# Optimization experiments

Measured on AMD Instinct MI355X. Metric: run time of the kernel, lower is better.

The kernel has to match this reference:

```python
import jax, jax.numpy as jnp
import numpy as np

# BERT-base geometry
B, N, H, DH = 4, 512, 12, 64
HID = H * DH            # 768
E = 65536               # total edges (~avg degree 32)
NREL = 64               # relation vocabulary


def setup_inputs() -> dict:
    key = jax.random.key(0)
    ks = jax.random.split(key, 12)
    node_states = jax.random.normal(ks[0], (B, N, HID), jnp.float32)
    b = jax.random.randint(ks[1], (E,), 0, B)
    hn = jax.random.randint(ks[2], (E,), 0, N)
    tn = jax.random.randint(ks[3], (E,), 0, N)
    r = jax.random.randint(ks[4], (E,), 0, NREL)
    edge_indices = jnp.stack([b, hn, tn, r]).astype(jnp.int32)  # (4, E)
    node_type_ids = jnp.zeros((B, N), jnp.int32)  # unused by this subclass
    sc = 0.02
    Wq = jax.random.normal(ks[5], (HID, HID), jnp.float32) * sc
    bq = jnp.zeros((HID,), jnp.float32)
    Wk = jax.random.normal(ks[6], (HID, HID), jnp.float32) * sc
    bk = jnp.zeros((HID,), jnp.float32)
    Wv = jax.random.normal(ks[7], (HID, HID), jnp.float32) * sc
    bv = jnp.zeros((HID,), jnp.float32)
    # relation matrix embeddings: one (DH, DH) matrix per relation id
    rel_emb = jnp.eye(DH, dtype=jnp.float32)[None] + jax.random.normal(ks[8], (NREL, DH, DH), jnp.float32) * sc
    return {"node_states": node_states, "edge_indices": edge_indices,
            "node_type_ids": node_type_ids, "Wq": Wq, "bq": bq,
            "Wk": Wk, "bk": bk, "Wv": Wv, "bv": bv, "rel_emb": rel_emb}


def reference(node_states, edge_indices, node_type_ids, Wq, bq, Wk, bk, Wv, bv, rel_emb):
    Bq, Nn, hid = node_states.shape
    # dense QKV projections (torch Linear: y = x @ W^T + b)
    Q = node_states @ Wq.T + bq
    K = node_states @ Wk.T + bk
    V = (node_states @ Wv.T + bv).reshape(Bq, Nn, H, DH)  # (B,N,H,D)
    be, he, te, re = edge_indices  # each (E,)
    # per-edge gathers
    Qe = Q[be, he].reshape(-1, H, DH)   # (E,H,D)
    Ke = K[be, te].reshape(-1, H, DH)   # (E,H,D)
    Re = rel_emb[re]                     # (E,D,D) relation matrix per edge
    # Q projected through relation matrix, then inner product with K per head
    Qp = jnp.einsum('ehd,edk->ehk', Qe, Re)
    logits = jnp.einsum('ehd,ehd->eh', Qp, Ke) / jnp.sqrt(jnp.float32(DH))  # (E,H)
    # sparse softmax over tail nodes: segment = (batch, head_node)
    seg = be * Nn + he
    nseg = Bq * Nn
    m = jax.ops.segment_max(logits, seg, num_segments=nseg)      # (BN,H)
    ex = jnp.exp(logits - m[seg])
    denom = jax.ops.segment_sum(ex, seg, num_segments=nseg)      # (BN,H)
    p = ex / denom[seg]                                          # (E,H)
    # dropout prob = 0.0 (deterministic reference)
    # aggregate: out[b,i,h,:] = sum_edges p_e * V[b, tail_e, h, :]
    contrib = p[:, :, None] * V[be, te]                          # (E,H,D)
    out = jax.ops.segment_sum(contrib, seg, num_segments=nseg)   # (BN,H,D)
    return out.reshape(Bq, Nn, H * DH)
```

## Files before the change

### kernel.cpp

```cpp
#include <hip/hip_runtime.h>
#include <hip/hip_bf16.h>

#define NB   4
#define NN   512
#define NH   12
#define DHD  64
#define HID  768
#define NE   65536
#define NSEG 2048
#define NREL 64
#define NSUB 32
#define NRSUB (NREL * NSUB)
#define LGS  16

typedef short bf16x8 __attribute__((ext_vector_type(8)));
typedef float f32x4  __attribute__((ext_vector_type(4)));

__device__ __forceinline__ unsigned short f2bf(float f) {
    __hip_bfloat16 h = __float2bfloat16(f);
    return *reinterpret_cast<unsigned short*>(&h);
}
__device__ __forceinline__ float bf2f(unsigned short s) {
    return __int_as_float(((int)s) << 16);
}
__device__ __forceinline__ void load_lds16(const void* g, void* l) {
    __builtin_amdgcn_global_load_lds(
        (const __attribute__((address_space(1))) unsigned int*)g,
        (__attribute__((address_space(3))) unsigned int*)l, 16, 0, 0);
}

#define NX4 ((2048 * 768) / 4)
#define NW4 ((768 * 768) / 4)
__global__ __launch_bounds__(256) void cast_kernel(
    const float* __restrict__ X, const float* __restrict__ Wq,
    const float* __restrict__ Wk, const float* __restrict__ Wv,
    unsigned short* __restrict__ Xh, unsigned short* __restrict__ Wh)
{
    const int i = blockIdx.x * 256 + threadIdx.x;
    float4 v;
    ushort4* dst;
    if (i < NX4) {
        v = ((const float4*)X)[i];
        dst = &((ushort4*)Xh)[i];
    } else {
        const int j = i - NX4;
        const float* W = (j < NW4) ? Wq : ((j < 2 * NW4) ? Wk : Wv);
        const int jj = (j < NW4) ? j : ((j < 2 * NW4) ? j - NW4 : j - 2 * NW4);
        v = ((const float4*)W)[jj];
        dst = &((ushort4*)Wh)[j];
    }
    ushort4 r;
    r.x = f2bf(v.x); r.y = f2bf(v.y); r.z = f2bf(v.z); r.w = f2bf(v.w);
    *dst = r;
}

__global__ __launch_bounds__(256) void qkv_mfma(
    const unsigned short* __restrict__ Xh, const unsigned short* __restrict__ Wh,
    const float* __restrict__ bq, const float* __restrict__ bk,
    const float* __restrict__ bv,
    unsigned short* __restrict__ Qh, unsigned short* __restrict__ Kh,
    float* __restrict__ Vo)
{
    const int z = blockIdx.z;
    const unsigned short* W = Wh + (size_t)z * (768 * 768);
    const float* bias = (z == 0) ? bq : ((z == 1) ? bk : bv);

    const int n0 = blockIdx.x * 128;
    const int m0 = blockIdx.y * 128;
    const int tid  = threadIdx.x;
    const int lane = tid & 63;
    const int wave = tid >> 6;
    const int wm = wave >> 1, wn = wave & 1;

    __shared__ unsigned short As[128 * 64];
    __shared__ unsigned short Bs[128 * 64];

    f32x4 acc[4][4];
    #pragma unroll
    for (int a = 0; a < 4; ++a)
        #pragma unroll
        for (int b = 0; b < 4; ++b) acc[a][b] = (f32x4){0.f, 0.f, 0.f, 0.f};

    const int ml = lane & 15;
    const int q4 = lane >> 4;

    for (int k0 = 0; k0 < HID; k0 += 64) {
        __syncthreads();
        #pragma unroll
        for (int l = 0; l < 4; ++l) {
            const int idx = (l * 4 + wave) * 64 + lane;
            const int row = idx >> 3;
            const int kq  = (idx & 7) ^ (row & 7);
            load_lds16(Xh + (size_t)(m0 + row) * HID + k0 + kq * 8,
                       As + (l * 4 + wave) * 512);
            load_lds16(W + (size_t)(n0 + row) * HID + k0 + kq * 8,
                       Bs + (l * 4 + wave) * 512);
        }
        __syncthreads();

        #pragma unroll
        for (int ks = 0; ks < 2; ++ks) {
            bf16x8 af[4], bfr[4];
            #pragma unroll
            for (int t = 0; t < 4; ++t) {
                const int ar = wm * 64 + t * 16 + ml;
                const int ac = (ks * 4 + q4) ^ (ar & 7);
                af[t] = *(const bf16x8*)(As + ar * 64 + ac * 8);
                const int br = wn * 64 + t * 16 + ml;
                const int bc = (ks * 4 + q4) ^ (br & 7);
                bfr[t] = *(const bf16x8*)(Bs + br * 64 + bc * 8);
            }
            #pragma unroll
            for (int mt = 0; mt < 4; ++mt)
                #pragma unroll
                for (int nt = 0; nt < 4; ++nt)
                    acc[mt][nt] = __builtin_amdgcn_mfma_f32_16x16x32_bf16(
                        af[mt], bfr[nt], acc[mt][nt], 0, 0, 0);
        }
    }

    #pragma unroll
    for (int nt = 0; nt < 4; ++nt) {
        const int col = n0 + wn * 64 + nt * 16 + ml;
        const float bcol = bias[col];
        #pragma unroll
        for (int mt = 0; mt < 4; ++mt) {
            const int row = m0 + wm * 64 + mt * 16 + q4 * 4;
            #pragma unroll
            for (int rg = 0; rg < 4; ++rg) {
                const float v = acc[mt][nt][rg] + bcol;
                const size_t o = (size_t)(row + rg) * HID + col;
                if (z == 0)      Qh[o] = f2bf(v);
                else if (z == 1) Kh[o] = f2bf(v);
                else             Vo[o] = v;
            }
        }
    }
}

__global__ void hist_kernel(const int* __restrict__ ei,
                            int* __restrict__ count, int* __restrict__ rcount2)
{
    const int e = blockIdx.x * 256 + threadIdx.x;
    const int b  = ei[e];
    const int hn = ei[NE + e];
    const int rr = ei[3 * NE + e];
    const int sub = (e >> 8) & (NSUB - 1);
    atomicAdd(&count[b * NN + hn], 1);
    atomicAdd(&rcount2[rr * NSUB + sub], 1);
}

__global__ void scan_kernel(const int* __restrict__ cnt, int* __restrict__ ofs)
{
    __shared__ int buf[256];
    const int tid = threadIdx.x;
    int local[8];
    int s = 0;
    #pragma unroll
    for (int i = 0; i < 8; ++i) { local[i] = cnt[tid * 8 + i]; s += local[i]; }
    buf[tid] = s;
    __syncthreads();
    for (int off = 1; off < 256; off <<= 1) {
        const int v = (tid >= off) ? buf[tid - off] : 0;
        __syncthreads();
        buf[tid] += v;
        __syncthreads();
    }
    int run = buf[tid] - s;
    #pragma unroll
    for (int i = 0; i < 8; ++i) { ofs[tid * 8 + i] = run; run += local[i]; }
    if (tid == 255) ofs[2048] = run;
}

__global__ void scatter_kernel(const int* __restrict__ ei, const int* __restrict__ offs,
                               int* __restrict__ cursor,
                               const int* __restrict__ rofs2, int* __restrict__ rcursor2,
                               int* __restrict__ s_te, int* __restrict__ s_seg,
                               int* __restrict__ r_pos)
{
    const int e = blockIdx.x * 256 + threadIdx.x;
    const int b  = ei[e];
    const int hn = ei[NE + e];
    const int tn = ei[2 * NE + e];
    const int rr = ei[3 * NE + e];
    const int sub = (e >> 8) & (NSUB - 1);
    const int seg = b * NN + hn;
    const int pos = offs[seg] + atomicAdd(&cursor[seg], 1);
    s_te[pos]  = tn;
    s_seg[pos] = seg;
    const int rb = rr * NSUB + sub;
    const int rj = atomicAdd(&rcursor2[rb], 1);
    r_pos[rofs2[rb] + rj] = pos;
}

__global__ __launch_bounds__(256) void rel_logits(
    const unsigned short* __restrict__ Qh, const unsigned short* __restrict__ Kh,
    const float* __restrict__ rel,
    const int* __restrict__ rofs2, const int* __restrict__ r_pos,
    const int* __restrict__ s_te, const int* __restrict__ s_seg,
    float* __restrict__ Lg)
{
    const int r = blockIdx.x;
    const int rstart = rofs2[r * NSUB];
    const int rows = (rofs2[(r + 1) * NSUB] - rstart) * NH;
    const int tid = threadIdx.x;
    const int lane = tid & 63;
    const int wave = tid >> 6;

    __shared__ float ReS[64][65];
    __shared__ int qb[256], kb[256], oi[256];
    __shared__ float QpS[4][16][67];

    {
        const float* Rg = rel + (size_t)r * 4096;
        for (int i = tid; i < 1024; i += 256) {
            const float4 v = ((const float4*)Rg)[i];
            const int row = i >> 4, c4 = (i & 15) * 4;
            ReS[row][c4] = v.x; ReS[row][c4 + 1] = v.y;
            ReS[row][c4 + 2] = v.z; ReS[row][c4 + 3] = v.w;
        }
    }
    __syncthreads();

    bf16x8 bfrag[2][4];
    {
        const int q4 = lane >> 4, n = lane & 15;
        #pragma unroll
        for (int ks = 0; ks < 2; ++ks)
            #pragma unroll
            for (int nt = 0; nt < 4; ++nt) {
                bf16x8 f;
                #pragma unroll
                for (int j = 0; j < 8; ++j)
                    f[j] = (short)f2bf(ReS[ks * 32 + q4 * 8 + j][nt * 16 + n]);
                bfrag[ks][nt] = f;
            }
    }

    for (int t0 = blockIdx.y * 256; t0 < rows; t0 += gridDim.y * 256) {
        __syncthreads();
        {
            const int rowid = t0 + tid;
            if (rowid < rows) {
                const int el = rowid / 12;
                const int h  = rowid - el * 12;
                const int pos = r_pos[rstart + el];
                const int seg = s_seg[pos];
                const int te  = s_te[pos];
                const int b   = seg >> 9;
                qb[tid] = seg * HID + h * 64;
                kb[tid] = (b * NN + te) * HID + h * 64;
                oi[tid] = pos * LGS + h;
            } else { qb[tid] = 0; kb[tid] = 0; oi[tid] = -1; }
        }
        __syncthreads();

        for (int g = wave; g < 16; g += 4) {
            const int m = lane & 15, q4 = lane >> 4;
            const int qbase = qb[g * 16 + m];
            f32x4 cfr[4] = {{0,0,0,0},{0,0,0,0},{0,0,0,0},{0,0,0,0}};
            #pragma unroll
            for (int ks = 0; ks < 2; ++ks) {
                const bf16x8 afr = *(const bf16x8*)(Qh + qbase + ks * 32 + q4 * 8);
                #pragma unroll
                for (int nt = 0; nt < 4; ++nt)
                    cfr[nt] = __builtin_amdgcn_mfma_f32_16x16x32_bf16(
                        afr, bfrag[ks][nt], cfr[nt], 0, 0, 0);
            }
            #pragma unroll
            for (int nt = 0; nt < 4; ++nt)
                #pragma unroll
                for (int rg = 0; rg < 4; ++rg)
                    QpS[wave][q4 * 4 + rg][nt * 16 + m] = cfr[nt][rg];

            const int rw = lane >> 2, ch = (lane & 3) * 16;
            const int rowid2 = g * 16 + rw;
            const int kbase = kb[rowid2];
            const bf16x8 k0 = *(const bf16x8*)(Kh + kbase + ch);
            const bf16x8 k1 = *(const bf16x8*)(Kh + kbase + ch + 8);
            float s = 0.f;
            #pragma unroll
            for (int i = 0; i < 8; ++i) {
                s = fmaf(QpS[wave][rw][ch + i],     bf2f((unsigned short)k0[i]), s);
                s = fmaf(QpS[wave][rw][ch + 8 + i], bf2f((unsigned short)k1[i]), s);
            }
            s += __shfl_xor(s, 1, 64);
            s += __shfl_xor(s, 2, 64);
            if ((lane & 3) == 0) {
                const int o = oi[rowid2];
                if (o >= 0) Lg[o] = s * 0.125f;
            }
        }
    }
}

__global__ __launch_bounds__(256) void seg_softmax_agg(
    const float* __restrict__ V, const float* __restrict__ Lg,
    const int* __restrict__ offs, const int* __restrict__ s_te,
    float* __restrict__ out)
{
    const int seg  = blockIdx.x;
    const int tid  = threadIdx.x;
    const int lane = tid & 63;
    const int w    = tid >> 6;
    const int start = offs[seg];
    const int cnt   = offs[seg + 1] - start;
    const int browbase = seg & ~(NN - 1);

    __shared__ int   te_s[64];
    __shared__ float pv[4][3][64];

    float m0 = -1e30f, m1 = -1e30f, m2 = -1e30f;
    float l0 = 0.f, l1 = 0.f, l2 = 0.f;
    float acc0 = 0.f, acc1 = 0.f, acc2 = 0.f;

    for (int c0 = 0; c0 < cnt; c0 += 64) {
        const int cc = min(64, cnt - c0);
        __syncthreads();
        if (tid < cc) te_s[tid] = s_te[start + c0 + tid];
        __syncthreads();

        float g0 = -1e30f, g1 = -1e30f, g2 = -1e30f;
        if (lane < cc) {
            const float* Lp = Lg + (size_t)(start + c0 + lane) * LGS;
            g0 = Lp[w]; g1 = Lp[4 + w]; g2 = Lp[8 + w];
        }
        float x0 = g0, x1 = g1, x2 = g2;
        #pragma unroll
        for (int o = 1; o < 64; o <<= 1) {
            x0 = fmaxf(x0, __shfl_xor(x0, o, 64));
            x1 = fmaxf(x1, __shfl_xor(x1, o, 64));
            x2 = fmaxf(x2, __shfl_xor(x2, o, 64));
        }
        const float nm0 = fmaxf(m0, x0), nm1 = fmaxf(m1, x1), nm2 = fmaxf(m2, x2);
        const float a0 = __expf(m0 - nm0), a1 = __expf(m1 - nm1), a2 = __expf(m2 - nm2);
        float p0 = (lane < cc) ? __expf(g0 - nm0) : 0.f;
        float p1 = (lane < cc) ? __expf(g1 - nm1) : 0.f;
        float p2 = (lane < cc) ? __expf(g2 - nm2) : 0.f;
        float s0 = p0, s1 = p1, s2 = p2;
        #pragma unroll
        for (int o = 1; o < 64; o <<= 1) {
            s0 += __shfl_xor(s0, o, 64);
            s1 += __shfl_xor(s1, o, 64);
            s2 += __shfl_xor(s2, o, 64);
        }
        l0 = l0 * a0 + s0; l1 = l1 * a1 + s1; l2 = l2 * a2 + s2;
        m0 = nm0; m1 = nm1; m2 = nm2;
        pv[w][0][lane] = p0; pv[w][1][lane] = p1; pv[w][2][lane] = p2;

        acc0 *= a0; acc1 *= a1; acc2 *= a2;
        for (int j = 0; j < cc; ++j) {
            const float* __restrict__ Vr =
                V + (size_t)(browbase + te_s[j]) * HID + lane;
            acc0 = fmaf(pv[w][0][j], Vr[w * 64],       acc0);
            acc1 = fmaf(pv[w][1][j], Vr[(4 + w) * 64], acc1);
            acc2 = fmaf(pv[w][2][j], Vr[(8 + w) * 64], acc2);
        }
    }

    float* Yo = out + (size_t)seg * HID;
    Yo[tid]       = (l0 > 0.f) ? acc0 / l0 : 0.f;
    Yo[tid + 256] = (l1 > 0.f) ? acc1 / l1 : 0.f;
    Yo[tid + 512] = (l2 > 0.f) ? acc2 / l2 : 0.f;
}

extern "C" void kernel_launch(void* const* d_in, const int* in_sizes, int n_in,
                              void* d_out, int out_size, void* d_ws, size_t ws_size,
                              hipStream_t stream)
{
    const float* X   = (const float*)d_in[0];
    const int*   EI  = (const int*)d_in[1];
    const float* Wq  = (const float*)d_in[3];
    const float* bq  = (const float*)d_in[4];
    const float* Wk  = (const float*)d_in[5];
    const float* bk  = (const float*)d_in[6];
    const float* Wv  = (const float*)d_in[7];
    const float* bv  = (const float*)d_in[8];
    const float* rel = (const float*)d_in[9];
    float* out = (float*)d_out;

    char* p = (char*)d_ws;
    unsigned short* Qh = (unsigned short*)p;  p += (size_t)NSEG * HID * 2;
    unsigned short* Kh = (unsigned short*)p;  p += (size_t)NSEG * HID * 2;
    float* Vb = (float*)p;                    p += (size_t)NSEG * HID * 4;
    unsigned short* Xh = (unsigned short*)p;
    float* Lg = (float*)p;                    p += (size_t)NE * LGS * 4;
    unsigned short* Wh = (unsigned short*)p;  p += (size_t)3 * 768 * 768 * 2;
    int* offs     = (int*)p;                  p += 2052 * 4;
    int* rofs2    = (int*)p;                  p += (NRSUB + 4) * 4;
    int* count    = (int*)p;                  p += NSEG * 4;
    int* cursor   = (int*)p;                  p += NSEG * 4;
    int* rcount2  = (int*)p;                  p += NRSUB * 4;
    int* rcursor2 = (int*)p;                  p += NRSUB * 4;
    int* s_te     = (int*)p;                  p += NE * 4;
    int* s_seg    = (int*)p;                  p += NE * 4;
    int* r_pos    = (int*)p;                  p += NE * 4;

    cast_kernel<<<(NX4 + 3 * NW4 + 255) / 256, 256, 0, stream>>>(
        X, Wq, Wk, Wv, Xh, Wh);
    qkv_mfma<<<dim3(HID / 128, (NB * NN) / 128, 3), 256, 0, stream>>>(
        Xh, Wh, bq, bk, bv, Qh, Kh, Vb);

    hipMemsetAsync(count, 0, (2 * NSEG + 2 * NRSUB) * sizeof(int), stream);
    hist_kernel<<<NE / 256, 256, 0, stream>>>(EI, count, rcount2);
    scan_kernel<<<1, 256, 0, stream>>>(count, offs);
    scan_kernel<<<1, 256, 0, stream>>>(rcount2, rofs2);
    scatter_kernel<<<NE / 256, 256, 0, stream>>>(EI, offs, cursor, rofs2, rcursor2,
                                                 s_te, s_seg, r_pos);

    rel_logits<<<dim3(NREL, 32), 256, 0, stream>>>(Qh, Kh, rel, rofs2, r_pos,
                                                   s_te, s_seg, Lg);
    seg_softmax_agg<<<NSEG, 256, 0, stream>>>(Vb, Lg, offs, s_te, out);
}
```

Baseline: 188.0 us.

## Fuse bf16 cast into QKV GEMM, merge scans, shuffle-based aggregation, retune grid

Removes the separate fp32-to-bf16 cast kernel and converts X and W tiles to bf16 while staging them into LDS inside the QKV GEMM. This drops a full read/write pass and one launch, but gives up async global_load_lds in favour of register-staged loads. The two scan launches become one two-block launch. The segment-softmax aggregation now broadcasts tail indices and probabilities with wave shuffles instead of LDS plus barriers. The rel_logits grid grows from 32 to 48 y-blocks, and the QpS row padding changes.

```diff
diff --git a/kernel.cpp b/kernel.cpp
--- a/kernel.cpp
+++ b/kernel.cpp
@@ -23,46 +23,18 @@
 __device__ __forceinline__ float bf2f(unsigned short s) {
     return __int_as_float(((int)s) << 16);
 }
-__device__ __forceinline__ void load_lds16(const void* g, void* l) {
-    __builtin_amdgcn_global_load_lds(
-        (const __attribute__((address_space(1))) unsigned int*)g,
-        (__attribute__((address_space(3))) unsigned int*)l, 16, 0, 0);
-}
-
-#define NX4 ((2048 * 768) / 4)
-#define NW4 ((768 * 768) / 4)
-__global__ __launch_bounds__(256) void cast_kernel(
-    const float* __restrict__ X, const float* __restrict__ Wq,
-    const float* __restrict__ Wk, const float* __restrict__ Wv,
-    unsigned short* __restrict__ Xh, unsigned short* __restrict__ Wh)
-{
-    const int i = blockIdx.x * 256 + threadIdx.x;
-    float4 v;
-    ushort4* dst;
-    if (i < NX4) {
-        v = ((const float4*)X)[i];
-        dst = &((ushort4*)Xh)[i];
-    } else {
-        const int j = i - NX4;
-        const float* W = (j < NW4) ? Wq : ((j < 2 * NW4) ? Wk : Wv);
-        const int jj = (j < NW4) ? j : ((j < 2 * NW4) ? j - NW4 : j - 2 * NW4);
-        v = ((const float4*)W)[jj];
-        dst = &((ushort4*)Wh)[j];
-    }
-    ushort4 r;
-    r.x = f2bf(v.x); r.y = f2bf(v.y); r.z = f2bf(v.z); r.w = f2bf(v.w);
-    *dst = r;
-}
 
 __global__ __launch_bounds__(256) void qkv_mfma(
-    const unsigned short* __restrict__ Xh, const unsigned short* __restrict__ Wh,
+    const float* __restrict__ X,
+    const float* __restrict__ Wq, const float* __restrict__ Wk,
+    const float* __restrict__ Wv,
     const float* __restrict__ bq, const float* __restrict__ bk,
     const float* __restrict__ bv,
     unsigned short* __restrict__ Qh, unsigned short* __restrict__ Kh,
     float* __restrict__ Vo)
 {
     const int z = blockIdx.z;
-    const unsigned short* W = Wh + (size_t)z * (768 * 768);
+    const float* W    = (z == 0) ? Wq : ((z == 1) ? Wk : Wv);
     const float* bias = (z == 0) ? bq : ((z == 1) ? bk : bv);
 
     const int n0 = blockIdx.x * 128;
@@ -87,14 +59,29 @@
     for (int k0 = 0; k0 < HID; k0 += 64) {
         __syncthreads();
         #pragma unroll
-        for (int l = 0; l < 4; ++l) {
-            const int idx = (l * 4 + wave) * 64 + lane;
+        for (int i = 0; i < 4; ++i) {
+            const int idx = tid + i * 256;
             const int row = idx >> 3;
-            const int kq  = (idx & 7) ^ (row & 7);
-            load_lds16(Xh + (size_t)(m0 + row) * HID + k0 + kq * 8,
-                       As + (l * 4 + wave) * 512);
-            load_lds16(W + (size_t)(n0 + row) * HID + k0 + kq * 8,
-                       Bs + (l * 4 + wave) * 512);
+            const int c   = idx & 7;
+            const int sl  = c ^ (row & 7);
+            const float* Xg = X + (size_t)(m0 + row) * HID + k0 + c * 8;
+            const float4 a0 = *(const float4*)Xg;
+            const float4 a1 = *(const float4*)(Xg + 4);
+            bf16x8 av;
+            av[0] = (short)f2bf(a0.x); av[1] = (short)f2bf(a0.y);
+            av[2] = (short)f2bf(a0.z); av[3] = (short)f2bf(a0.w);
+            av[4] = (short)f2bf(a1.x); av[5] = (short)f2bf(a1.y);
+            av[6] = (short)f2bf(a1.z); av[7] = (short)f2bf(a1.w);
+            *(bf16x8*)&As[row * 64 + sl * 8] = av;
+            const float* Wg = W + (size_t)(n0 + row) * HID + k0 + c * 8;
+            const float4 b0 = *(const float4*)Wg;
+            const float4 b1 = *(const float4*)(Wg + 4);
+            bf16x8 bv8;
+            bv8[0] = (short)f2bf(b0.x); bv8[1] = (short)f2bf(b0.y);
+            bv8[2] = (short)f2bf(b0.z); bv8[3] = (short)f2bf(b0.w);
+            bv8[4] = (short)f2bf(b1.x); bv8[5] = (short)f2bf(b1.y);
+            bv8[6] = (short)f2bf(b1.z); bv8[7] = (short)f2bf(b1.w);
+            *(bf16x8*)&Bs[row * 64 + sl * 8] = bv8;
         }
         __syncthreads();
 
@@ -150,8 +137,11 @@
     atomicAdd(&rcount2[rr * NSUB + sub], 1);
 }
 
-__global__ void scan_kernel(const int* __restrict__ cnt, int* __restrict__ ofs)
-{
+__global__ void scan2_kernel(const int* __restrict__ cntA, int* __restrict__ ofsA,
+                             const int* __restrict__ cntB, int* __restrict__ ofsB)
+{
+    const int* cnt = blockIdx.x ? cntB : cntA;
+    int* ofs       = blockIdx.x ? ofsB : ofsA;
     __shared__ int buf[256];
     const int tid = threadIdx.x;
     int local[8];
@@ -193,6 +183,7 @@
     r_pos[rofs2[rb] + rj] = pos;
 }
 
+#define RLY 48
 __global__ __launch_bounds__(256) void rel_logits(
     const unsigned short* __restrict__ Qh, const unsigned short* __restrict__ Kh,
     const float* __restrict__ rel,
@@ -209,7 +200,7 @@
 
     __shared__ float ReS[64][65];
     __shared__ int qb[256], kb[256], oi[256];
-    __shared__ float QpS[4][16][67];
+    __shared__ float QpS[4][16][68];
 
     {
         const float* Rg = rel + (size_t)r * 4096;
@@ -237,7 +228,7 @@
             }
     }
 
-    for (int t0 = blockIdx.y * 256; t0 < rows; t0 += gridDim.y * 256) {
+    for (int t0 = blockIdx.y * 256; t0 < rows; t0 += RLY * 256) {
         __syncthreads();
         {
             const int rowid = t0 + tid;
@@ -307,21 +298,17 @@
     const int cnt   = offs[seg + 1] - start;
     const int browbase = seg & ~(NN - 1);
 
-    __shared__ int   te_s[64];
-    __shared__ float pv[4][3][64];
-
     float m0 = -1e30f, m1 = -1e30f, m2 = -1e30f;
     float l0 = 0.f, l1 = 0.f, l2 = 0.f;
     float acc0 = 0.f, acc1 = 0.f, acc2 = 0.f;
 
     for (int c0 = 0; c0 < cnt; c0 += 64) {
         const int cc = min(64, cnt - c0);
-        __syncthreads();
-        if (tid < cc) te_s[tid] = s_te[start + c0 + tid];
-        __syncthreads();
-
+
+        int te = 0;
         float g0 = -1e30f, g1 = -1e30f, g2 = -1e30f;
         if (lane < cc) {
+            te = s_te[start + c0 + lane];
             const float* Lp = Lg + (size_t)(start + c0 + lane) * LGS;
             g0 = Lp[w]; g1 = Lp[4 + w]; g2 = Lp[8 + w];
         }
@@ -334,9 +321,9 @@
         }
         const float nm0 = fmaxf(m0, x0), nm1 = fmaxf(m1, x1), nm2 = fmaxf(m2, x2);
         const float a0 = __expf(m0 - nm0), a1 = __expf(m1 - nm1), a2 = __expf(m2 - nm2);
-        float p0 = (lane < cc) ? __expf(g0 - nm0) : 0.f;
-        float p1 = (lane < cc) ? __expf(g1 - nm1) : 0.f;
-        float p2 = (lane < cc) ? __expf(g2 - nm2) : 0.f;
+        const float p0 = (lane < cc) ? __expf(g0 - nm0) : 0.f;
+        const float p1 = (lane < cc) ? __expf(g1 - nm1) : 0.f;
+        const float p2 = (lane < cc) ? __expf(g2 - nm2) : 0.f;
         float s0 = p0, s1 = p1, s2 = p2;
         #pragma unroll
         for (int o = 1; o < 64; o <<= 1) {
@@ -346,15 +333,14 @@
         }
         l0 = l0 * a0 + s0; l1 = l1 * a1 + s1; l2 = l2 * a2 + s2;
         m0 = nm0; m1 = nm1; m2 = nm2;
-        pv[w][0][lane] = p0; pv[w][1][lane] = p1; pv[w][2][lane] = p2;
 
         acc0 *= a0; acc1 *= a1; acc2 *= a2;
         for (int j = 0; j < cc; ++j) {
-            const float* __restrict__ Vr =
-                V + (size_t)(browbase + te_s[j]) * HID + lane;
-            acc0 = fmaf(pv[w][0][j], Vr[w * 64],       acc0);
-            acc1 = fmaf(pv[w][1][j], Vr[(4 + w) * 64], acc1);
-            acc2 = fmaf(pv[w][2][j], Vr[(8 + w) * 64], acc2);
+            const int row = browbase + __shfl(te, j, 64);
+            const float* __restrict__ Vr = V + (size_t)row * HID + lane;
+            acc0 = fmaf(__shfl(p0, j, 64), Vr[w * 64],       acc0);
+            acc1 = fmaf(__shfl(p1, j, 64), Vr[(4 + w) * 64], acc1);
+            acc2 = fmaf(__shfl(p2, j, 64), Vr[(8 + w) * 64], acc2);
         }
     }
 
@@ -383,9 +369,7 @@
     unsigned short* Qh = (unsigned short*)p;  p += (size_t)NSEG * HID * 2;
     unsigned short* Kh = (unsigned short*)p;  p += (size_t)NSEG * HID * 2;
     float* Vb = (float*)p;                    p += (size_t)NSEG * HID * 4;
-    unsigned short* Xh = (unsigned short*)p;
     float* Lg = (float*)p;                    p += (size_t)NE * LGS * 4;
-    unsigned short* Wh = (unsigned short*)p;  p += (size_t)3 * 768 * 768 * 2;
     int* offs     = (int*)p;                  p += 2052 * 4;
     int* rofs2    = (int*)p;                  p += (NRSUB + 4) * 4;
     int* count    = (int*)p;                  p += NSEG * 4;
@@ -396,19 +380,16 @@
     int* s_seg    = (int*)p;                  p += NE * 4;
     int* r_pos    = (int*)p;                  p += NE * 4;
 
-    cast_kernel<<<(NX4 + 3 * NW4 + 255) / 256, 256, 0, stream>>>(
-        X, Wq, Wk, Wv, Xh, Wh);
     qkv_mfma<<<dim3(HID / 128, (NB * NN) / 128, 3), 256, 0, stream>>>(
-        Xh, Wh, bq, bk, bv, Qh, Kh, Vb);
+        X, Wq, Wk, Wv, bq, bk, bv, Qh, Kh, Vb);
 
     hipMemsetAsync(count, 0, (2 * NSEG + 2 * NRSUB) * sizeof(int), stream);
     hist_kernel<<<NE / 256, 256, 0, stream>>>(EI, count, rcount2);
-    scan_kernel<<<1, 256, 0, stream>>>(count, offs);
-    scan_kernel<<<1, 256, 0, stream>>>(rcount2, rofs2);
+    scan2_kernel<<<2, 256, 0, stream>>>(count, offs, rcount2, rofs2);
     scatter_kernel<<<NE / 256, 256, 0, stream>>>(EI, offs, cursor, rofs2, rcursor2,
                                                  s_te, s_seg, r_pos);
 
-    rel_logits<<<dim3(NREL, 32), 256, 0, stream>>>(Qh, Kh, rel, rofs2, r_pos,
-                                                   s_te, s_seg, Lg);
+    rel_logits<<<dim3(NREL, RLY), 256, 0, stream>>>(Qh, Kh, rel, rofs2, r_pos,
+                                                    s_te, s_seg, Lg);
     seg_softmax_agg<<<NSEG, 256, 0, stream>>>(Vb, Lg, offs, s_te, out);
 }
```

New measurement: 199.6 us. 1.06x slower.
